# Kernel tuning notes

Measured on AMD Instinct MI355X. Metric: run time of the kernel, lower is better.

Reference implementation:

```python
import jax, jax.numpy as jnp
import numpy as np

B, A, C, M = 32, 8400, 80, 32
TOP_K, ALPHA, BETA, EPS = 13, 1.0, 6.0, 1e-9


def _boxes(key, shape):
    # valid xyxy boxes in a 640x640 image
    u = jax.random.uniform(key, shape, jnp.float32)
    xy = u[..., :2] * 640.0
    wh = u[..., 2:] * 128.0 + 2.0
    return jnp.concatenate([xy, xy + wh], axis=-1)


def setup_inputs() -> dict:
    key = jax.random.key(0)
    k = jax.random.split(key, 6)
    pd_scores = jax.random.uniform(k[0], (B, A, C), jnp.float32)
    pd_bboxes = _boxes(k[1], (B, A, 4))
    anc_points = jax.random.uniform(k[2], (A, 2), jnp.float32) * 640.0
    gt_labels = jax.random.randint(k[3], (B, M, 1), 0, C, jnp.int32)
    gt_bboxes = _boxes(k[4], (B, M, 4))
    mask_gt = (jax.random.uniform(k[5], (B, M, 1)) < 0.8).astype(jnp.float32)
    return {"pd_scores": pd_scores, "pd_bboxes": pd_bboxes, "anc_points": anc_points,
            "gt_labels": gt_labels, "gt_bboxes": gt_bboxes, "mask_gt": mask_gt}


def _assign(pd_scores, pd_bboxes, anc_points, gt_labels, gt_bboxes, mask_gt):
    b, a, nc = pd_scores.shape
    m = gt_bboxes.shape[1]
    dtype = pd_scores.dtype

    # --- candidate anchors inside each GT box: (B, M, A) ---
    lt, rb = gt_bboxes[..., :2], gt_bboxes[..., 2:]                  # (B,M,2)
    deltas = jnp.concatenate([anc_points[None, None] - lt[:, :, None],
                              rb[:, :, None] - anc_points[None, None]], axis=-1)  # (B,M,A,4)
    mask_in_gts = (deltas.min(-1) > EPS).astype(dtype)               # (B,M,A)
    gt_mask = (mask_in_gts * mask_gt) > 0                            # bool (B,M,A)

    # --- classification score of each anchor for its GT's class ---
    labels = gt_labels[..., 0].astype(jnp.int32)                     # (B,M)
    scores_tc = jnp.swapaxes(pd_scores, 1, 2)                        # (B,C,A)
    idx = jnp.broadcast_to(labels[:, :, None], (b, m, a))
    bbox_scores = jnp.take_along_axis(scores_tc, idx, axis=1)        # (B,M,A)
    bbox_scores = jnp.where(gt_mask, bbox_scores, 0.0)

    # --- pairwise IoU gt x pred: (B,M,A) ---
    lt_i = jnp.maximum(gt_bboxes[:, :, None, :2], pd_bboxes[:, None, :, :2])
    rb_i = jnp.minimum(gt_bboxes[:, :, None, 2:], pd_bboxes[:, None, :, 2:])
    wh = jnp.clip(rb_i - lt_i, 0.0)
    inter = wh[..., 0] * wh[..., 1]
    area_g = ((gt_bboxes[..., 2] - gt_bboxes[..., 0]) * (gt_bboxes[..., 3] - gt_bboxes[..., 1]))[:, :, None]
    area_p = ((pd_bboxes[..., 2] - pd_bboxes[..., 0]) * (pd_bboxes[..., 3] - pd_bboxes[..., 1]))[:, None, :]
    iou = inter / (area_g + area_p - inter + EPS)
    overlaps = jnp.clip(jnp.where(gt_mask, iou, 0.0), 0.0)

    align_metric = bbox_scores ** ALPHA * overlaps ** BETA           # (B,M,A)

    # --- top-k over anchors, dedup via scatter-add counts ---
    tk_vals, tk_idx = jax.lax.top_k(align_metric, TOP_K)             # (B,M,K)
    tk_mask = jnp.broadcast_to(mask_gt > 0, (b, m, TOP_K))
    tk_idx = jnp.where(tk_mask, tk_idx, 0)
    bi = jnp.arange(b)[:, None, None]
    mi = jnp.arange(m)[None, :, None]
    counts = jnp.zeros((b, m, a), jnp.int32).at[bi, mi, tk_idx].add(1)
    mask_top_k = jnp.where(counts > 1, 0, counts).astype(dtype)

    mask_pos = mask_top_k * mask_in_gts * mask_gt                    # (B,M,A)
    fg_mask = mask_pos.sum(1)                                        # (B,A)

    # --- resolve anchors assigned to multiple GTs by max IoU ---
    # (always applied; identical to torch's conditional branch when no conflicts)
    mask_multi = jnp.broadcast_to(fg_mask[:, None, :] > 1, (b, m, a))
    max_ov_idx = jnp.argmax(overlaps, axis=1)                        # (B,A)
    is_max = (max_ov_idx[:, None, :] == jnp.arange(m)[None, :, None]).astype(dtype)
    mask_pos = jnp.where(mask_multi, is_max, mask_pos)
    fg_mask = mask_pos.sum(1)

    # --- gather targets ---
    tgt_idx = jnp.argmax(mask_pos, axis=1)                           # (B,A)
    tgt_labels = jnp.clip(jnp.take_along_axis(labels, tgt_idx, axis=1), 0)  # (B,A)
    tgt_bboxes = jnp.take_along_axis(gt_bboxes, jnp.broadcast_to(tgt_idx[:, :, None], (b, a, 4)), axis=1)

    one_hot = (tgt_labels[..., None] == jnp.arange(nc)).astype(dtype)  # (B,A,C)
    target_scores = one_hot * (fg_mask > 0)[..., None].astype(dtype)

    # --- normalize scores by aligned metric ---
    am = align_metric * mask_pos
    pos_am = am.max(-1, keepdims=True)                               # (B,M,1)
    pos_ov = (overlaps * mask_pos).max(-1, keepdims=True)            # (B,M,1)
    norm = (am * pos_ov / (pos_am + EPS)).max(axis=1)[..., None]     # (B,A,1)
    target_scores = target_scores * norm

    return tgt_bboxes, target_scores, fg_mask > 0


def reference(pd_scores, pd_bboxes, anc_points, gt_labels, gt_bboxes, mask_gt):
    return _assign(pd_scores, pd_bboxes, anc_points, gt_labels, gt_bboxes, mask_gt)
```

## Files before the change

### kernel.cpp

```cpp
#include <hip/hip_runtime.h>

#define Bq 32
#define Aq 8400
#define Cq 80
#define Mq 32
#define TOPK 13
#define CAP 512
#define NW (Mq * TOPK)
#define EPSq 1e-9f

__device__ __forceinline__ bool better(float v1, int i1, float v2, int i2) {
    return (v1 > v2) || ((v1 == v2) && (i1 < i2));
}

__device__ __forceinline__ float iou4(float4 g, float4 p, float garea) {
    float ix1 = fmaxf(g.x, p.x), iy1 = fmaxf(g.y, p.y);
    float ix2 = fminf(g.z, p.z), iy2 = fminf(g.w, p.w);
    float iw = fmaxf(ix2 - ix1, 0.f), ih = fmaxf(iy2 - iy1, 0.f);
    float inter = iw * ih;
    float parea = (p.z - p.x) * (p.w - p.y);
    return inter / (((garea + parea) - inter) + EPSq);
}

__device__ __forceinline__ float in_min4(float ax, float ay, float4 g) {
    return fminf(fminf(ax - g.x, ay - g.y), fminf(g.z - ax, g.w - ay));
}

__device__ __forceinline__ void ins13(float (&val)[TOPK], int (&idx)[TOPK], float al, int a) {
    if (better(al, a, val[TOPK - 1], idx[TOPK - 1])) {
        #pragma unroll
        for (int k = TOPK - 1; k >= 1; --k) {
            bool bk   = better(val[k],     idx[k],     al, a);
            bool bkm1 = better(val[k - 1], idx[k - 1], al, a);
            val[k] = bk ? val[k] : (bkm1 ? al : val[k - 1]);
            idx[k] = bk ? idx[k] : (bkm1 ? a  : idx[k - 1]);
        }
        bool b0 = better(val[0], idx[0], al, a);
        val[0] = b0 ? val[0] : al;
        idx[0] = b0 ? idx[0] : a;
    }
}

__global__ __launch_bounds__(256) void k_build(
    const float* __restrict__ pd_scores, const float* __restrict__ pd_bboxes,
    const float* __restrict__ anc, const int* __restrict__ gt_labels,
    const float* __restrict__ gt_bboxes, const float* __restrict__ mask_gt,
    int* __restrict__ winners)
{
    int m = blockIdx.x, b = blockIdx.y;
    int t = threadIdx.x, lane = t & 63;

    __shared__ int   s_n;
    __shared__ int   s_list[CAP];
    __shared__ float s_val[CAP];

    if (mask_gt[b * Mq + m] <= 0.f) {
        if (t < TOPK) winners[(b * Mq + m) * TOPK + t] = -1;
        return;
    }

    if (t == 0) s_n = 0;
    __syncthreads();

    float4 gb = ((const float4*)gt_bboxes)[b * Mq + m];
    float garea = (gb.z - gb.x) * (gb.w - gb.y);

    for (int a = t; a < Aq; a += 256) {
        float2 ap = ((const float2*)anc)[a];
        bool in = in_min4(ap.x, ap.y, gb) > EPSq;
        unsigned long long bal = __ballot(in);
        if (bal) {
            int rank = __popcll(bal & ((1ull << lane) - 1ull));
            int leader = __ffsll(bal) - 1;
            int base = 0;
            if (lane == leader) base = atomicAdd(&s_n, (int)__popcll(bal));
            base = __shfl(base, leader);
            int pos = base + rank;
            if (in && pos < CAP) s_list[pos] = a;
        }
    }
    __syncthreads();

    int n = s_n < CAP ? s_n : CAP;
    int lbl = gt_labels[b * Mq + m];
    for (int e = t; e < n; e += 256) {
        int a = s_list[e];
        float4 pb = ((const float4*)pd_bboxes)[(size_t)b * Aq + a];
        float ov = fmaxf(iou4(gb, pb, garea), 0.f);
        float sc = pd_scores[((size_t)b * Aq + a) * Cq + lbl];
        float o2 = ov * ov;
        s_val[e] = sc * (o2 * o2 * o2);
    }
    __syncthreads();

    if (t >= 64) return;

    float val[TOPK]; int idx[TOPK];
    #pragma unroll
    for (int k = 0; k < TOPK; k++) { val[k] = -1.f; idx[k] = 0x7fffffff; }

    {
        float2 apl = ((const float2*)anc)[lane];
        if (!(in_min4(apl.x, apl.y, gb) > EPSq)) ins13(val, idx, 0.f, lane);
    }
    for (int e = lane; e < n; e += 64) ins13(val, idx, s_val[e], s_list[e]);

    int win_i = 0x7fffffff;
    #pragma unroll
    for (int r = 0; r < TOPK; ++r) {
        float bv = val[0]; int bi = idx[0];
        #pragma unroll
        for (int off = 1; off < 64; off <<= 1) {
            float ovv = __shfl_xor(bv, off);
            int   oii = __shfl_xor(bi, off);
            if (better(ovv, oii, bv, bi)) { bv = ovv; bi = oii; }
        }
        if (lane == r) win_i = bi;
        if (idx[0] == bi) {
            #pragma unroll
            for (int k = 0; k < TOPK - 1; ++k) { val[k] = val[k + 1]; idx[k] = idx[k + 1]; }
            val[TOPK - 1] = -1.f; idx[TOPK - 1] = 0x7fffffff;
        }
    }
    if (lane < TOPK) {
        int outv = -1;
        if (win_i < Aq) {
            float2 ap = ((const float2*)anc)[win_i];
            if (in_min4(ap.x, ap.y, gb) > EPSq) outv = win_i;
        }
        winners[(b * Mq + m) * TOPK + lane] = outv;
    }
}

__global__ __launch_bounds__(256) void k_write(
    const float* __restrict__ pd_scores, const float* __restrict__ pd_bboxes,
    const float* __restrict__ anc, const int* __restrict__ gt_labels,
    const float* __restrict__ gt_bboxes, const float* __restrict__ mask_gt,
    const int* __restrict__ winners,
    float* __restrict__ out_bboxes, float* __restrict__ out_scores,
    float* __restrict__ out_fg)
{
    int b = blockIdx.y;
    int a0 = blockIdx.x * 256;
    int t = threadIdx.x;

    __shared__ unsigned int smask[Aq];
    __shared__ unsigned int s_am[Mq], s_ov[Mq];
    __shared__ float4 sgb[Mq];
    __shared__ int    slbl[Mq];
    __shared__ int    smv[Mq];
    __shared__ float  snv[256];
    __shared__ int    slb[256];

    if (t < Mq) {
        sgb[t]  = ((const float4*)gt_bboxes)[b * Mq + t];
        slbl[t] = gt_labels[b * Mq + t];
        smv[t]  = (mask_gt[b * Mq + t] > 0.f) ? 1 : 0;
        s_am[t] = 0u; s_ov[t] = 0u;
    }
    for (int a = t; a < Aq; a += 256) smask[a] = 0u;
    __syncthreads();

    for (int e = t; e < NW; e += 256) {
        int a = winners[(size_t)b * NW + e];
        if (a >= 0) atomicOr(&smask[a], 1u << (e / TOPK));
    }
    __syncthreads();

    int ea[2]; unsigned int ewm[2];
    #pragma unroll
    for (int r = 0; r < 2; ++r) {
        int e = t + r * 256;
        int a = (e < NW) ? winners[(size_t)b * NW + e] : -1;
        ea[r] = a;
        ewm[r] = (a >= 0) ? smask[a] : 0u;
    }
    __syncthreads();

    #pragma unroll
    for (int r = 0; r < 2; ++r) {
        int a = ea[r];
        if (a < 0) continue;
        unsigned int w = ewm[r];
        float4 pb = ((const float4*)pd_bboxes)[(size_t)b * Aq + a];
        float2 ap = ((const float2*)anc)[a];
        if (__popc(w) > 1) {
            float bv = -1.f; int bj = 0;
            for (int mm = 0; mm < Mq; mm++) {
                float4 g = sgb[mm];
                float ov = 0.f;
                if (in_min4(ap.x, ap.y, g) > EPSq && smv[mm]) {
                    float garea = (g.z - g.x) * (g.w - g.y);
                    ov = fmaxf(iou4(g, pb, garea), 0.f);
                }
                if (ov > bv) { bv = ov; bj = mm; }
            }
            w = 1u << bj;
            smask[a] = w;
        }
        int j = __ffs(w) - 1;
        float al = 0.f, ov = 0.f;
        float4 g = sgb[j];
        if (in_min4(ap.x, ap.y, g) > EPSq && smv[j]) {
            float garea = (g.z - g.x) * (g.w - g.y);
            ov = fmaxf(iou4(g, pb, garea), 0.f);
            float sc = pd_scores[((size_t)b * Aq + a) * Cq + slbl[j]];
            float o2 = ov * ov;
            al = sc * (o2 * o2 * o2);
        }
        atomicMax(&s_am[j], __float_as_uint(al));
        atomicMax(&s_ov[j], __float_as_uint(ov));
    }
    __syncthreads();

    int a = a0 + t;
    {
        float nv = 0.f; int lb = -1;
        if (a < Aq) {
            size_t i = (size_t)b * Aq + a;
            unsigned int w = smask[a];
            int j = w ? (__ffs(w) - 1) : 0;
            ((float4*)out_bboxes)[i] = sgb[j];
            out_fg[i] = w ? 1.f : 0.f;
            if (w) {
                lb = slbl[j];
                float2 ap = ((const float2*)anc)[a];
                float4 pb = ((const float4*)pd_bboxes)[i];
                float al = 0.f;
                float4 g = sgb[j];
                if (in_min4(ap.x, ap.y, g) > EPSq && smv[j]) {
                    float garea = (g.z - g.x) * (g.w - g.y);
                    float ov = fmaxf(iou4(g, pb, garea), 0.f);
                    float sc = pd_scores[i * Cq + lb];
                    float o2 = ov * ov;
                    al = sc * (o2 * o2 * o2);
                }
                float pam = __uint_as_float(s_am[j]);
                float pov = __uint_as_float(s_ov[j]);
                nv = al * pov / (pam + EPSq);
            }
        }
        snv[t] = nv;
        slb[t] = lb;
    }
    __syncthreads();

    const int C4 = Cq / 4;
    int nrow = Aq - a0; if (nrow > 256) nrow = 256;
    for (int idx = t; idx < nrow * C4; idx += 256) {
        int row = idx / C4, c4 = idx - row * C4;
        float4 o = make_float4(0.f, 0.f, 0.f, 0.f);
        int lbr = slb[row];
        if (lbr >= 0 && (lbr >> 2) == c4) {
            float v = snv[row];
            int p = lbr & 3;
            if (p == 0) o.x = v; else if (p == 1) o.y = v;
            else if (p == 2) o.z = v; else o.w = v;
        }
        ((float4*)out_scores)[((size_t)b * Aq + a0 + row) * C4 + c4] = o;
    }
}

extern "C" void kernel_launch(void* const* d_in, const int* in_sizes, int n_in,
                              void* d_out, int out_size, void* d_ws, size_t ws_size,
                              hipStream_t stream) {
    const float* pd_scores = (const float*)d_in[0];
    const float* pd_bboxes = (const float*)d_in[1];
    const float* anc       = (const float*)d_in[2];
    const int*   gt_labels = (const int*)d_in[3];
    const float* gt_bboxes = (const float*)d_in[4];
    const float* mask_gt   = (const float*)d_in[5];

    float* out_bboxes = (float*)d_out;
    float* out_scores = out_bboxes + (size_t)Bq * Aq * 4;
    float* out_fg     = out_scores + (size_t)Bq * Aq * Cq;

    int* winners = (int*)d_ws;

    k_build<<<dim3(Mq, Bq), 256, 0, stream>>>(
        pd_scores, pd_bboxes, anc, gt_labels, gt_bboxes, mask_gt, winners);

    k_write<<<dim3((Aq + 255) / 256, Bq), 256, 0, stream>>>(
        pd_scores, pd_bboxes, anc, gt_labels, gt_bboxes, mask_gt, winners,
        out_bboxes, out_scores, out_fg);
}
```

Measured before the change: 190.3 us.

## Split per-image mask resolution into a separate kernel to remove redundant block work

The per-image winner mask construction, multi-GT conflict resolution and per-GT max reductions were repeated by every anchor-tile block. They now run once per image in a 1024-thread kernel that writes a packed (normalized value, GT index, fg flag) record per anchor to workspace. A new output kernel reads this record to emit bboxes, fg and one-hot scores. This adds a kernel launch, extra workspace traffic, and a low-parallelism stage with only one block per image.

```diff
diff --git a/kernel.cpp b/kernel.cpp
--- a/kernel.cpp
+++ b/kernel.cpp
@@ -132,16 +132,14 @@
     }
 }
 
-__global__ __launch_bounds__(256) void k_write(
+__global__ __launch_bounds__(1024) void k_img(
     const float* __restrict__ pd_scores, const float* __restrict__ pd_bboxes,
     const float* __restrict__ anc, const int* __restrict__ gt_labels,
     const float* __restrict__ gt_bboxes, const float* __restrict__ mask_gt,
     const int* __restrict__ winners,
-    float* __restrict__ out_bboxes, float* __restrict__ out_scores,
-    float* __restrict__ out_fg)
+    uint2* __restrict__ packed)
 {
-    int b = blockIdx.y;
-    int a0 = blockIdx.x * 256;
+    int b = blockIdx.x;
     int t = threadIdx.x;
 
     __shared__ unsigned int smask[Aq];
@@ -149,8 +147,6 @@
     __shared__ float4 sgb[Mq];
     __shared__ int    slbl[Mq];
     __shared__ int    smv[Mq];
-    __shared__ float  snv[256];
-    __shared__ int    slb[256];
 
     if (t < Mq) {
         sgb[t]  = ((const float4*)gt_bboxes)[b * Mq + t];
@@ -158,30 +154,19 @@
         smv[t]  = (mask_gt[b * Mq + t] > 0.f) ? 1 : 0;
         s_am[t] = 0u; s_ov[t] = 0u;
     }
-    for (int a = t; a < Aq; a += 256) smask[a] = 0u;
-    __syncthreads();
-
-    for (int e = t; e < NW; e += 256) {
-        int a = winners[(size_t)b * NW + e];
-        if (a >= 0) atomicOr(&smask[a], 1u << (e / TOPK));
-    }
-    __syncthreads();
-
-    int ea[2]; unsigned int ewm[2];
-    #pragma unroll
-    for (int r = 0; r < 2; ++r) {
-        int e = t + r * 256;
-        int a = (e < NW) ? winners[(size_t)b * NW + e] : -1;
-        ea[r] = a;
-        ewm[r] = (a >= 0) ? smask[a] : 0u;
-    }
-    __syncthreads();
-
-    #pragma unroll
-    for (int r = 0; r < 2; ++r) {
-        int a = ea[r];
-        if (a < 0) continue;
-        unsigned int w = ewm[r];
+    for (int a = t; a < Aq; a += 1024) smask[a] = 0u;
+    __syncthreads();
+
+    int ea = (t < NW) ? winners[(size_t)b * NW + t] : -1;
+    if (ea >= 0) atomicOr(&smask[ea], 1u << (t / TOPK));
+    __syncthreads();
+
+    unsigned int ewm = (ea >= 0) ? smask[ea] : 0u;
+    __syncthreads();
+
+    if (ea >= 0) {
+        int a = ea;
+        unsigned int w = ewm;
         float4 pb = ((const float4*)pd_bboxes)[(size_t)b * Aq + a];
         float2 ap = ((const float2*)anc)[a];
         if (__popc(w) > 1) {
@@ -213,32 +198,63 @@
     }
     __syncthreads();
 
+    for (int a = t; a < Aq; a += 1024) {
+        unsigned int w = smask[a];
+        int j = w ? (__ffs(w) - 1) : 0;
+        float nv = 0.f;
+        if (w) {
+            float2 ap = ((const float2*)anc)[a];
+            float4 pb = ((const float4*)pd_bboxes)[(size_t)b * Aq + a];
+            float al = 0.f;
+            float4 g = sgb[j];
+            if (in_min4(ap.x, ap.y, g) > EPSq && smv[j]) {
+                float garea = (g.z - g.x) * (g.w - g.y);
+                float ov = fmaxf(iou4(g, pb, garea), 0.f);
+                float sc = pd_scores[((size_t)b * Aq + a) * Cq + slbl[j]];
+                float o2 = ov * ov;
+                al = sc * (o2 * o2 * o2);
+            }
+            float pam = __uint_as_float(s_am[j]);
+            float pov = __uint_as_float(s_ov[j]);
+            nv = al * pov / (pam + EPSq);
+        }
+        packed[(size_t)b * Aq + a] = make_uint2(__float_as_uint(nv),
+                                               ((unsigned int)j << 1) | (w ? 1u : 0u));
+    }
+}
+
+__global__ __launch_bounds__(256) void k_out(
+    const int* __restrict__ gt_labels, const float* __restrict__ gt_bboxes,
+    const uint2* __restrict__ packed,
+    float* __restrict__ out_bboxes, float* __restrict__ out_scores,
+    float* __restrict__ out_fg)
+{
+    int b = blockIdx.y;
+    int a0 = blockIdx.x * 256;
+    int t = threadIdx.x;
+
+    __shared__ float4 sgb[Mq];
+    __shared__ int    slbl[Mq];
+    __shared__ float  snv[256];
+    __shared__ int    slb[256];
+
+    if (t < Mq) {
+        sgb[t]  = ((const float4*)gt_bboxes)[b * Mq + t];
+        slbl[t] = gt_labels[b * Mq + t];
+    }
+    __syncthreads();
+
     int a = a0 + t;
     {
         float nv = 0.f; int lb = -1;
         if (a < Aq) {
             size_t i = (size_t)b * Aq + a;
-            unsigned int w = smask[a];
-            int j = w ? (__ffs(w) - 1) : 0;
+            uint2 p = packed[i];
+            int j = (int)(p.y >> 1);
+            bool fg = (p.y & 1u) != 0u;
             ((float4*)out_bboxes)[i] = sgb[j];
-            out_fg[i] = w ? 1.f : 0.f;
-            if (w) {
-                lb = slbl[j];
-                float2 ap = ((const float2*)anc)[a];
-                float4 pb = ((const float4*)pd_bboxes)[i];
-                float al = 0.f;
-                float4 g = sgb[j];
-                if (in_min4(ap.x, ap.y, g) > EPSq && smv[j]) {
-                    float garea = (g.z - g.x) * (g.w - g.y);
-                    float ov = fmaxf(iou4(g, pb, garea), 0.f);
-                    float sc = pd_scores[i * Cq + lb];
-                    float o2 = ov * ov;
-                    al = sc * (o2 * o2 * o2);
-                }
-                float pam = __uint_as_float(s_am[j]);
-                float pov = __uint_as_float(s_ov[j]);
-                nv = al * pov / (pam + EPSq);
-            }
+            out_fg[i] = fg ? 1.f : 0.f;
+            if (fg) { nv = __uint_as_float(p.x); lb = slbl[j]; }
         }
         snv[t] = nv;
         slb[t] = lb;
@@ -275,12 +291,16 @@
     float* out_scores = out_bboxes + (size_t)Bq * Aq * 4;
     float* out_fg     = out_scores + (size_t)Bq * Aq * Cq;
 
-    int* winners = (int*)d_ws;
+    char* ws = (char*)d_ws;
+    int*   winners = (int*)ws;            ws += (size_t)Bq * Mq * TOPK * 4;
+    uint2* packed  = (uint2*)ws;          ws += (size_t)Bq * Aq * 8;
 
     k_build<<<dim3(Mq, Bq), 256, 0, stream>>>(
         pd_scores, pd_bboxes, anc, gt_labels, gt_bboxes, mask_gt, winners);
 
-    k_write<<<dim3((Aq + 255) / 256, Bq), 256, 0, stream>>>(
-        pd_scores, pd_bboxes, anc, gt_labels, gt_bboxes, mask_gt, winners,
-        out_bboxes, out_scores, out_fg);
-}
+    k_img<<<dim3(Bq), 1024, 0, stream>>>(
+        pd_scores, pd_bboxes, anc, gt_labels, gt_bboxes, mask_gt, winners, packed);
+
+    k_out<<<dim3((Aq + 255) / 256, Bq), 256, 0, stream>>>(
+        gt_labels, gt_bboxes, packed, out_bboxes, out_scores, out_fg);
+}
```

New measurement: 193.6 us. Within noise of the previous version (+1.7%).
